# Kernel optimization log

Hardware: AMD Instinct MI355X
Metric: run time of the kernel (lower is better)

The kernel has to match this reference:

```python
import jax, jax.numpy as jnp
import numpy as np
from jax import lax

# Module hyperparameters (match init_kwargs / torch defaults)
VMIN, VMAX = 0, 255
LEVELS = 8
KS = 5          # kernel_size (box filter)
POOL = 32       # avg-pool size/stride
DISTANCES = np.linspace(1, 1, 1)            # distanceCount=1
ANGLES = np.linspace(0, 360, 8 + 1)[:-1]    # angleCount=8 -> 0,45,...,315 deg
L2 = LEVELS * LEVELS


def setup_inputs() -> dict:
    key = jax.random.key(0)
    # pixel intensities in [0, 255)
    x = jax.random.uniform(key, (2, 1, 256, 256), dtype=jnp.float32) * 255.0
    return {"x": x}


def _shift_nearest(gl1, dx, dy):
    # kornia warp_affine with M=[[1,0,-dx],[0,1,-dy]], nearest, border padding
    # is dst(x,y) = src(x+dx, y+dy) with round-to-nearest and edge clamping.
    b, c, h, w = gl1.shape
    xi = jnp.clip(jnp.round(jnp.arange(w) + dx).astype(jnp.int32), 0, w - 1)
    yi = jnp.clip(jnp.round(jnp.arange(h) + dy).astype(jnp.int32), 0, h - 1)
    return gl1[:, :, yi[:, None], xi[None, :]]


def _glcm(x, distance, angle_deg):
    # torch.bucketize(x, bins) - 1  ==  searchsorted(bins, x, 'left') - 1
    bins = jnp.linspace(VMIN, VMAX + 1, LEVELS + 1)
    gl1 = jnp.searchsorted(bins, x, side='left') - 1          # (b,c,h,w) int
    rad = np.deg2rad(angle_deg)
    dx = distance * np.cos(rad)
    dy = -distance * np.sin(rad)   # original uses sin(-angle)
    gl2 = _shift_nearest(gl1, dx, dy)
    # fused co-occurrence code: one value per pixel in [0, L2)
    code = gl1 * LEVELS + gl2                                  # (b,c,h,w)
    onehot = (code[..., None] == jnp.arange(L2)).astype(jnp.float32)  # (b,c,h,w,L2)
    # kornia filter2d: ones KSxKS kernel, reflect border, unnormalized sum
    p = KS // 2
    yp = jnp.pad(onehot, ((0, 0), (0, 0), (p, p), (p, p), (0, 0)), mode='reflect')
    filt = lax.reduce_window(yp, 0.0, lax.add,
                             (1, 1, KS, KS, 1), (1, 1, 1, 1, 1), 'VALID')
    # view(L2,b,c,h,w).permute(1,0,2,3,4) -> (b, L2, c, h, w)
    return jnp.transpose(filt, (0, 4, 1, 2, 3))


def reference(x):
    b, c, h, w = x.shape
    glcms = []
    for distance in DISTANCES:
        per_angle = [_glcm(x, float(distance), float(a)) for a in ANGLES]
        glcms.append(jnp.stack(per_angle, axis=1))   # (b, A, L2, c, h, w)
    g = jnp.stack(glcms, axis=1)                      # (b, D, A, L2, c, h, w)
    g = g.reshape(b, -1, h, w)                        # (b, D*A*L2*c, h, w)
    # AvgPool2d(POOL, stride=POOL)
    pooled = lax.reduce_window(g, 0.0, lax.add,
                               (1, 1, POOL, POOL), (1, 1, POOL, POOL), 'VALID')
    return pooled / float(POOL * POOL)
```

## Files before the change

kernel.cpp:

```cpp
#include <hip/hip_runtime.h>


#define POOLSZ 32
#define PADR   2
#define H      256
#define W      256
#define NLEV   8
#define NCODE  64
#define NANG   8
#define TILE   38
#define NWAVE  4

__device__ __forceinline__ int reflect_idx(int t) {
    if (t < 0)   return -t;
    if (t > 255) return 510 - t;
    return t;
}

__global__ __launch_bounds__(256) void glcm_kernel(const float* __restrict__ x,
                                                   float* __restrict__ out) {
    const int bid = blockIdx.x;
    const int a   = bid & 7;
    const int px  = (bid >> 3) & 7;
    const int py  = (bid >> 6) & 7;
    const int b   = bid >> 9;

    __shared__ signed char gl[TILE][TILE];
    __shared__ float wrow[TILE];
    __shared__ float wcol[TILE];
    __shared__ float hist4[NWAVE * NCODE];

    const int tid = threadIdx.x;
    const int wid = tid >> 6;

    hist4[tid] = 0.0f;

    const int row0 = py * POOLSZ - 3;
    const int col0 = px * POOLSZ - 3;

    if (wid < 3) {
        const float* xb = x + b * (H * W);
        for (int i = tid; i < TILE * TILE; i += 192) {
            int ly = i / TILE, lx = i % TILE;
            int gy = min(max(row0 + ly, 0), H - 1);
            int gx = min(max(col0 + lx, 0), W - 1);
            float v = xb[gy * W + gx];
            gl[ly][lx] = (signed char)((int)ceilf(v * 0.03125f) - 1);
        }
    } else {
        for (int j = tid - 192; j < 2 * TILE; j += 64) {
            int dim = j / TILE;
            int l   = j % TILE;
            int o   = dim ? col0 : row0;
            int p   = dim ? px : py;
            int lo  = p * POOLSZ, hi = lo + POOLSZ - 1;
            int s_abs = o + l;
            int wgt = 0;
            if (s_abs >= 0 && s_abs <= 255) {
                for (int t = lo - PADR; t <= hi + PADR; ++t) {
                    if (reflect_idx(t) == s_abs) {
                        wgt += min(t + PADR, hi) - max(t - PADR, lo) + 1;
                    }
                }
            }
            if (dim) wcol[l] = (float)wgt; else wrow[l] = (float)wgt;
        }
    }
    __syncthreads();

    const int offy_t[8] = {0, -1, -1, -1, 0, 1, 1, 1};
    const int offx_t[8] = {1,  1,  0, -1, -1, -1, 0, 1};
    const int offy = offy_t[a], offx = offx_t[a];

    float* myhist = &hist4[wid * NCODE];
    for (int i = tid; i < 36 * 36; i += 256) {
        int ly = i / 36 + 1;
        int lx = i % 36 + 1;
        float w = wrow[ly] * wcol[lx];
        int g1 = gl[ly][lx];
        int g2 = gl[ly + offy][lx + offx];
        int code = g1 * NLEV + g2;
        if (w != 0.0f && code >= 0) atomicAdd(&myhist[code], w);
    }
    __syncthreads();

    if (tid < NCODE) {
        float s = hist4[tid] + hist4[NCODE + tid] + hist4[2 * NCODE + tid]
                + hist4[3 * NCODE + tid];
        float* ob = out + ((size_t)(b * (NANG * NCODE) + a * NCODE) * 64) + py * 8 + px;
        ob[(size_t)tid * 64] = s * (1.0f / 1024.0f);
    }
}

extern "C" void kernel_launch(void* const* d_in, const int* in_sizes, int n_in,
                              void* d_out, int out_size, void* d_ws, size_t ws_size,
                              hipStream_t stream) {
    const float* x = (const float*)d_in[0];
    float* out = (float*)d_out;
    glcm_kernel<<<dim3(2 * 8 * 8 * 8), dim3(256), 0, stream>>>(x, out);
}
```

Measured before the change: 61.70 us.

## Split pool windows into row strips and compute all angles per block

```diff
diff --git a/kernel.cpp b/kernel.cpp
--- a/kernel.cpp
+++ b/kernel.cpp
@@ -2,13 +2,15 @@
 
 
 #define POOLSZ 32
-#define PADR   2
 #define H      256
 #define W      256
 #define NLEV   8
 #define NCODE  64
 #define NANG   8
-#define TILE   38
+#define SR     6
+#define NSTRIP 6
+#define SROWS  (SR + 2)
+#define TW     38
 #define NWAVE  4
 
 __device__ __forceinline__ int reflect_idx(int t) {
@@ -19,76 +21,78 @@
 
 __global__ __launch_bounds__(256) void glcm_kernel(const float* __restrict__ x,
                                                    float* __restrict__ out) {
-    const int bid = blockIdx.x;
-    const int a   = bid & 7;
-    const int px  = (bid >> 3) & 7;
-    const int py  = (bid >> 6) & 7;
-    const int b   = bid >> 9;
+    const int s  = blockIdx.x;
+    const int px = blockIdx.y & 7;
+    const int py = blockIdx.y >> 3;
+    const int b  = blockIdx.z;
 
-    __shared__ signed char gl[TILE][TILE];
-    __shared__ float wrow[TILE];
-    __shared__ float wcol[TILE];
-    __shared__ float hist4[NWAVE * NCODE];
+    __shared__ int   gl[SROWS][TW];
+    __shared__ float wrowS[SROWS];
+    __shared__ float wcol[TW];
+    __shared__ float hist4[NWAVE * NANG * NCODE];
 
     const int tid = threadIdx.x;
     const int wid = tid >> 6;
 
-    hist4[tid] = 0.0f;
+    const int row0 = py * POOLSZ - 3 + s * SR;
+    const int col0 = px * POOLSZ - 3;
 
-    const int row0 = py * POOLSZ - 3;
-    const int col0 = px * POOLSZ - 3;
+    for (int i = tid; i < NWAVE * NANG * NCODE; i += 256) hist4[i] = 0.0f;
 
     if (wid < 3) {
         const float* xb = x + b * (H * W);
-        for (int i = tid; i < TILE * TILE; i += 192) {
-            int ly = i / TILE, lx = i % TILE;
+        for (int i = tid; i < SROWS * TW; i += 192) {
+            int ly = i / TW, lx = i % TW;
             int gy = min(max(row0 + ly, 0), H - 1);
             int gx = min(max(col0 + lx, 0), W - 1);
             float v = xb[gy * W + gx];
-            gl[ly][lx] = (signed char)((int)ceilf(v * 0.03125f) - 1);
+            gl[ly][lx] = (int)ceilf(v * 0.03125f) - 1;
         }
     } else {
-        for (int j = tid - 192; j < 2 * TILE; j += 64) {
-            int dim = j / TILE;
-            int l   = j % TILE;
-            int o   = dim ? col0 : row0;
-            int p   = dim ? px : py;
+        for (int j = tid - 192; j < TW + SROWS; j += 64) {
+            int dim = (j >= TW);
+            int l   = dim ? (j - TW) : j;
+            int o   = dim ? row0 : col0;
+            int p   = dim ? py : px;
             int lo  = p * POOLSZ, hi = lo + POOLSZ - 1;
             int s_abs = o + l;
             int wgt = 0;
             if (s_abs >= 0 && s_abs <= 255) {
-                for (int t = lo - PADR; t <= hi + PADR; ++t) {
-                    if (reflect_idx(t) == s_abs) {
-                        wgt += min(t + PADR, hi) - max(t - PADR, lo) + 1;
-                    }
+                for (int t = lo - 2; t <= hi + 2; ++t) {
+                    if (reflect_idx(t) == s_abs)
+                        wgt += min(t + 2, hi) - max(t - 2, lo) + 1;
                 }
             }
-            if (dim) wcol[l] = (float)wgt; else wrow[l] = (float)wgt;
+            if (dim) wrowS[l] = (float)wgt; else wcol[l] = (float)wgt;
         }
     }
     __syncthreads();
 
     const int offy_t[8] = {0, -1, -1, -1, 0, 1, 1, 1};
     const int offx_t[8] = {1,  1,  0, -1, -1, -1, 0, 1};
-    const int offy = offy_t[a], offx = offx_t[a];
 
-    float* myhist = &hist4[wid * NCODE];
-    for (int i = tid; i < 36 * 36; i += 256) {
+    float* myh = &hist4[wid * (NANG * NCODE)];
+    for (int i = tid; i < SR * 36; i += 256) {
         int ly = i / 36 + 1;
         int lx = i % 36 + 1;
-        float w = wrow[ly] * wcol[lx];
-        int g1 = gl[ly][lx];
-        int g2 = gl[ly + offy][lx + offx];
-        int code = g1 * NLEV + g2;
-        if (w != 0.0f && code >= 0) atomicAdd(&myhist[code], w);
+        float w = wrowS[ly] * wcol[lx];
+        if (w == 0.0f) continue;
+        int g1   = gl[ly][lx];
+        int base = g1 * NLEV;
+        #pragma unroll
+        for (int a = 0; a < NANG; ++a) {
+            int g2   = gl[ly + offy_t[a]][lx + offx_t[a]];
+            int code = base + g2;
+            if (code >= 0) atomicAdd(&myh[a * NCODE + code], w);
+        }
     }
     __syncthreads();
 
-    if (tid < NCODE) {
-        float s = hist4[tid] + hist4[NCODE + tid] + hist4[2 * NCODE + tid]
-                + hist4[3 * NCODE + tid];
-        float* ob = out + ((size_t)(b * (NANG * NCODE) + a * NCODE) * 64) + py * 8 + px;
-        ob[(size_t)tid * 64] = s * (1.0f / 1024.0f);
+    for (int k = tid; k < NANG * NCODE; k += 256) {
+        float v = hist4[k] + hist4[512 + k] + hist4[1024 + k] + hist4[1536 + k];
+        if (v != 0.0f)
+            atomicAdd(&out[(size_t)(b * 512 + k) * 64 + py * 8 + px],
+                      v * (1.0f / 1024.0f));
     }
 }
 
@@ -97,5 +101,6 @@
                               hipStream_t stream) {
     const float* x = (const float*)d_in[0];
     float* out = (float*)d_out;
-    glcm_kernel<<<dim3(2 * 8 * 8 * 8), dim3(256), 0, stream>>>(x, out);
+    hipMemsetAsync(d_out, 0, (size_t)out_size, stream);
+    glcm_kernel<<<dim3(NSTRIP, 64, 2), dim3(256), 0, stream>>>(x, out);
 }
```

Measured after the change: 78.20 us. +26.8%, slower.
